# Optimization experiments

Measured on AMD Instinct MI355X. Metric: run time of the kernel, lower is better.

The kernel has to match this reference:

```python
import jax, jax.numpy as jnp
import numpy as np

U, V = 208, 176  # hard-coded DFT output shape from the original DFT2D
B, C, KH, KW = 32, 8, 3, 3


def dft2d(p):
    """Faithful vectorization of the original nested-loop DFT2D.
    dft[l, k] = (1/(M*N)) * sum_{m,n} p[m,n] * exp(-2j*pi*(k*m/V + l*n/U)),
    output shape (U, V) = (208, 176). Note the (intentionally) non-standard
    normalization axes, copied exactly from the source.
    """
    M, N = p.shape
    km = jnp.outer(jnp.arange(V), jnp.arange(M)).astype(jnp.float32)  # (V, M)
    ln = jnp.outer(jnp.arange(U), jnp.arange(N)).astype(jnp.float32)  # (U, N)
    E1 = jnp.exp(-2j * jnp.pi * km / V)  # (V, M) complex64
    E2 = jnp.exp(-2j * jnp.pi * ln / U)  # (U, N) complex64
    return jnp.einsum('km,mn,ln->lk', E1, p.astype(jnp.complex64), E2) / (M * N)


def setup_inputs() -> dict:
    key = jax.random.key(0)
    k1, k2 = jax.random.split(key)
    x = jax.random.normal(k1, (B, C, U, V), dtype=jnp.float32)
    kernel = jax.random.normal(k2, (KH, KW, 1, 1), dtype=jnp.float32)
    bias = jnp.zeros((1,), dtype=jnp.float32)
    return {"x": x, "kernel": kernel, "bias": bias}


def reference(x, kernel, bias):
    # Build the symmetric spatial kernel: [[k, flip_h(k)], [flip_w(k), flip_hw(k)]]
    k2 = kernel[::-1, :, :, :]
    k3 = kernel[:, ::-1, :, :]
    k4 = kernel[::-1, ::-1, :, :]
    sk = jnp.concatenate([jnp.concatenate([kernel, k2], axis=0),
                          jnp.concatenate([k3, k4], axis=0)], axis=1)  # (2KH, 2KW, 1, 1)
    sk2d = sk[:, :, 0, 0]  # tf.squeeze -> (2KH, 2KW)

    # k-space representation of the kernel and 50th-percentile binary mask
    fft_k = dft2d(sk2d)  # (208, 176) complex
    r = jnp.real(fft_k)
    thr = jnp.percentile(r, 50.0, method='nearest')  # tfp.stats.percentile default
    mask = (r > thr).astype(jnp.float32)  # (208, 176)

    # FFT of the image over its innermost two dims, mask in k-space, inverse FFT
    fft_x = jnp.fft.fft2(x)  # (B, C, 208, 176) complex64
    out = jnp.abs(jnp.fft.ifft2(fft_x * mask))  # bias unused on the test path
    return out
```

## Files before the change

kernel.cpp:

```cpp
#include <hip/hip_runtime.h>
#include <math.h>

#define UU 208
#define VV 176
#define NPIX (UU*VV)
#define ROWBLKS 1664

typedef __attribute__((ext_vector_type(2))) float v2f;
typedef __attribute__((ext_vector_type(4))) float v4f;

__device__ __forceinline__ v2f mk2(float x, float y){ v2f r; r.x = x; r.y = y; return r; }
__device__ __forceinline__ v2f sp(float s){ v2f r; r.x = s; r.y = s; return r; }

template<bool INV>
__device__ __forceinline__ v2f cmulc(v2f a, float wx, float wy_fwd){
  const float wy = INV ? -wy_fwd : wy_fwd;
  return sp(a.x) * mk2(wx, wy) + sp(a.y) * mk2(-wy, wx);
}
__device__ __forceinline__ v2f cmulw4(v2f a, v4f t){
  return sp(a.x) * mk2(t.x, t.y) + sp(a.y) * mk2(t.z, t.w);
}
__device__ __forceinline__ v2f cmulw4i(v2f a, v4f t){
  return sp(a.x) * mk2(t.x, t.z) + sp(a.y) * mk2(t.y, t.w);
}

template<bool INV>
__device__ __forceinline__ void dft4(v2f& x0, v2f& x1, v2f& x2, v2f& x3){
  v2f s0 = x0 + x2, d0 = x0 - x2;
  v2f s1 = x1 + x3, d1 = x1 - x3;
  v2f jd1;
  if (INV){ jd1.x = -d1.y; jd1.y =  d1.x; }
  else    { jd1.x =  d1.y; jd1.y = -d1.x; }
  x0 = s0 + s1; x2 = s0 - s1;
  x1 = d0 + jd1; x3 = d0 - jd1;
}

template<bool INV>
__device__ __forceinline__ void fft16(v2f v[16]){
  dft4<INV>(v[0], v[4], v[8],  v[12]);
  dft4<INV>(v[1], v[5], v[9],  v[13]);
  dft4<INV>(v[2], v[6], v[10], v[14]);
  dft4<INV>(v[3], v[7], v[11], v[15]);
  const float C1 = 0.92387953251128674f;
  const float S1 = 0.38268343236508978f;
  const float R2 = 0.70710678118654752f;
  v[5]  = cmulc<INV>(v[5],  C1, -S1);
  v[9]  = cmulc<INV>(v[9],  R2, -R2);
  v[13] = cmulc<INV>(v[13], S1, -C1);
  v[6]  = cmulc<INV>(v[6],  R2, -R2);
  v[10] = cmulc<INV>(v[10], 0.f, -1.f);
  v[14] = cmulc<INV>(v[14], -R2, -R2);
  v[7]  = cmulc<INV>(v[7],  S1, -C1);
  v[11] = cmulc<INV>(v[11], -R2, -R2);
  v[15] = cmulc<INV>(v[15], -C1,  S1);
  dft4<INV>(v[0],  v[1],  v[2],  v[3]);
  dft4<INV>(v[4],  v[5],  v[6],  v[7]);
  dft4<INV>(v[8],  v[9],  v[10], v[11]);
  dft4<INV>(v[12], v[13], v[14], v[15]);
}

template<int N, bool INV>
__device__ __forceinline__ void dftN(const v2f* __restrict__ t, v2f* __restrict__ F,
                                     const v2f* __restrict__ cs){
  v2f a = t[0];
  #pragma unroll
  for (int n = 1; n < N; n++) a += t[n];
  F[0] = a;
  #pragma unroll
  for (int k = 1; k <= N/2; k++){
    v2f C = t[0], S = sp(0.f);
    #pragma unroll
    for (int n = 1; n < N; n++){
      const int idx = (n * k) % N;
      C += t[n] * sp(cs[idx].x);
      S += t[n] * sp(cs[idx].y);
    }
    v2f ssw; ssw.x = S.y; ssw.y = -S.x;
    if (!INV){ F[k] = C + ssw; F[N-k] = C - ssw; }
    else     { F[k] = C - ssw; F[N-k] = C + ssw; }
  }
}

__device__ __forceinline__ unsigned sortable(float f){
  unsigned u = __float_as_uint(f);
  return (u & 0x80000000u) ? ~u : (u | 0x80000000u);
}

__device__ __forceinline__ unsigned find_bucket(const unsigned* __restrict__ bins_g,
                                                unsigned* sWS, unsigned* sB, unsigned* sK){
  const int t = threadIdx.x, lane = t & 63, wv = t >> 6;
  unsigned c = bins_g[t];
  unsigned v = c;
  #pragma unroll
  for (int d = 1; d < 64; d <<= 1){
    unsigned u = __shfl_up(v, d, 64);
    if (lane >= d) v += u;
  }
  if (lane == 63) sWS[wv] = v;
  __syncthreads();
  unsigned woff = 0;
  #pragma unroll
  for (int j = 0; j < 3; j++) woff += (j < wv) ? sWS[j] : 0u;
  unsigned incl = v + woff, excl = incl - c;
  unsigned k = *sK;
  __syncthreads();
  if (k >= excl && k < incl){ *sB = (unsigned)t; *sK = k - excl; }
  __syncthreads();
  return *sB;
}

__global__ __launch_bounds__(256) void rowfft_mask(const float* __restrict__ x, v2f* __restrict__ freq,
                                                   const float* __restrict__ kin, float* __restrict__ rbuf,
                                                   unsigned* __restrict__ bins24){
  const double PI2 = 6.283185307179586476925286766559;
  __shared__ v4f wf[VV];
  __shared__ v2f cs11[11];
  __shared__ v2f mid[16][177];
  if (blockIdx.x >= ROWBLKS){
    unsigned* h = (unsigned*)mid;
    h[threadIdx.x] = 0u;
    int i = (blockIdx.x - ROWBLKS) * 256 + threadIdx.x;
    int l = i / VV, k = i - l * VV;
    double c1, s1, c2, s2;
    { double a = PI2 * (double)k / (double)VV; c1 = cos(a); s1 = sin(a); }
    { double a = PI2 * (double)l / (double)UU; c2 = cos(a); s2 = sin(a); }
    double cA[6], sA[6], cB[6], sB[6];
    cA[0] = 1.0; sA[0] = 0.0; cA[1] = c1; sA[1] = s1;
    cB[0] = 1.0; sB[0] = 0.0; cB[1] = c2; sB[1] = s2;
    #pragma unroll
    for (int m = 2; m < 6; m++){
      cA[m] = 2.0*c1*cA[m-1] - cA[m-2];
      sA[m] = 2.0*c1*sA[m-1] - sA[m-2];
      cB[m] = 2.0*c2*cB[m-1] - cB[m-2];
      sB[m] = 2.0*c2*sB[m-1] - sB[m-2];
    }
    const int rm[6] = {0, 1, 2, 2, 1, 0};
    double P[3], Q[3];
    #pragma unroll
    for (int a = 0; a < 3; a++){
      P[a] = 0.0; Q[a] = 0.0;
      #pragma unroll
      for (int n = 0; n < 6; n++){
        double kv = (double)kin[a*3 + rm[n]];
        P[a] += kv * cB[n];
        Q[a] += kv * sB[n];
      }
    }
    double s = 0.0;
    #pragma unroll
    for (int m = 0; m < 6; m++)
      s += cA[m]*P[rm[m]] - sA[m]*Q[rm[m]];
    float val = (float)(s / 36.0);
    rbuf[i] = val;
    __syncthreads();
    atomicAdd(&h[sortable(val) >> 24], 1u);
    __syncthreads();
    if (h[threadIdx.x]) atomicAdd(&bins24[threadIdx.x], h[threadIdx.x]);
    return;
  }
  { int i = threadIdx.x;
    if (i < VV){
      double a = -PI2 * (double)i / (double)VV;
      float c = (float)cos(a), s = (float)sin(a);
      v4f f; f.x = c; f.y = s; f.z = -s; f.w = c; wf[i] = f;
    }
    if (i < 11){
      double a = PI2 * (double)i / 11.0;
      cs11[i] = mk2((float)cos(a), (float)sin(a));
    } }
  const int gr = threadIdx.x >> 4, ln = threadIdx.x & 15;
  const int row = blockIdx.x * 16 + gr;
  const int p = row / UU, rr = row - p * UU;
  const float* xr1 = x + ((size_t)(2*p) * UU + rr) * VV;
  const float* xr2 = xr1 + (size_t)NPIX;
  v2f* fr = freq + (size_t)row * VV;
  __syncthreads();
  if (ln < 11){
    v2f v[16];
    #pragma unroll
    for (int a = 0; a < 16; a++) v[a] = mk2(xr1[11*a + ln], xr2[11*a + ln]);
    fft16<false>(v);
    #pragma unroll
    for (int j = 0; j < 16; j++)
      mid[gr][j*11 + ln] = cmulw4(v[4*(j&3) + (j>>2)], wf[ln*j]);
  }
  v2f t[11], F[11];
  #pragma unroll
  for (int n2 = 0; n2 < 11; n2++) t[n2] = mid[gr][ln*11 + n2];
  dftN<11,false>(t, F, cs11);
  #pragma unroll
  for (int k2 = 0; k2 < 11; k2++) fr[ln + 16*k2] = F[k2];
}

template<int LEVEL>
__global__ __launch_bounds__(256) void hist_pass(const float* __restrict__ rbuf,
                                                 const unsigned* __restrict__ binsAll,
                                                 unsigned* __restrict__ binsOut){
  __shared__ unsigned h[256];
  __shared__ unsigned sWS[4];
  __shared__ unsigned sB, sK;
  if (threadIdx.x == 0) sK = 18304u;
  h[threadIdx.x] = 0u;
  __syncthreads();
  unsigned prefix = find_bucket(binsAll, sWS, &sB, &sK) << 24;
  if (LEVEL >= 2) prefix |= find_bucket(binsAll + 256, sWS, &sB, &sK) << 16;
  if (LEVEL >= 3) prefix |= find_bucket(binsAll + 512, sWS, &sB, &sK) << 8;
  const int SHIFT = 24 - 8*LEVEL;
  int i = blockIdx.x * 256 + threadIdx.x;
  unsigned u = sortable(rbuf[i]);
  if ((u >> (SHIFT + 8)) == (prefix >> (SHIFT + 8)))
    atomicAdd(&h[(u >> SHIFT) & 255u], 1u);
  __syncthreads();
  if (h[threadIdx.x]) atomicAdd(&binsOut[threadIdx.x], h[threadIdx.x]);
}

__global__ __launch_bounds__(256) void thr_final(const unsigned* __restrict__ binsAll,
                                                 float* __restrict__ thrOut){
  __shared__ unsigned sWS[4];
  __shared__ unsigned sB, sK;
  if (threadIdx.x == 0) sK = 18304u;
  __syncthreads();
  unsigned prefix = find_bucket(binsAll,       sWS, &sB, &sK) << 24;
  prefix |= find_bucket(binsAll + 256, sWS, &sB, &sK) << 16;
  prefix |= find_bucket(binsAll + 512, sWS, &sB, &sK) << 8;
  prefix |= find_bucket(binsAll + 768, sWS, &sB, &sK);
  if (threadIdx.x == 0){
    unsigned u = prefix;
    u = (u & 0x80000000u) ? (u ^ 0x80000000u) : ~u;
    thrOut[0] = __uint_as_float(u);
  }
}

__global__ __launch_bounds__(256) void colfft(v2f* __restrict__ freq,
                                              const float* __restrict__ rbuf, const float* __restrict__ thrp){
  __shared__ v4f wf[UU];
  __shared__ v2f cs13[13];
  __shared__ v2f buf[UU*17];
  { int i = threadIdx.x;
    const double PI2 = 6.283185307179586476925286766559;
    if (i < UU){
      double a = -PI2 * (double)i / (double)UU;
      float c = (float)cos(a), s = (float)sin(a);
      v4f f; f.x = c; f.y = s; f.z = -s; f.w = c; wf[i] = f;
    }
    if (i < 13){
      double a = PI2 * (double)i / 13.0;
      cs13[i] = mk2((float)cos(a), (float)sin(a));
    } }
  const int role = threadIdx.x >> 4, c = threadIdx.x & 15;
  const int img = blockIdx.x / 11;
  const int v0 = (blockIdx.x - img*11) << 4;
  v2f* base = freq + (size_t)img * NPIX + v0 + c;
  const float thr = thrp[0];
  __syncthreads();
  if (role < 13){
    v2f v[16];
    #pragma unroll
    for (int a = 0; a < 16; a++) v[a] = base[(13*a + role)*VV];
    fft16<false>(v);
    #pragma unroll
    for (int j = 0; j < 16; j++)
      buf[(j*13 + role)*17 + c] = cmulw4(v[4*(j&3) + (j>>2)], wf[role*j]);
  }
  __syncthreads();
  v2f F[13];
  {
    v2f t[13];
    #pragma unroll
    for (int n2 = 0; n2 < 13; n2++) t[n2] = buf[(role*13 + n2)*17 + c];
    dftN<13,false>(t, F, cs13);
    #pragma unroll
    for (int k2 = 0; k2 < 13; k2++){
      int u = role + 16*k2;
      float m = (rbuf[u*VV + v0 + c] > thr) ? 1.0f : 0.0f;
      F[k2] *= sp(m);
    }
  }
  __syncthreads();
  #pragma unroll
  for (int k2 = 0; k2 < 13; k2++) buf[(role + 16*k2)*17 + c] = F[k2];
  __syncthreads();
  if (role < 13){
    v2f v[16];
    #pragma unroll
    for (int a = 0; a < 16; a++) v[a] = buf[(13*a + role)*17 + c];
    fft16<true>(v);
    #pragma unroll
    for (int j = 0; j < 16; j++)
      buf[(j*13 + role)*17 + c] = cmulw4i(v[4*(j&3) + (j>>2)], wf[role*j]);
  }
  __syncthreads();
  {
    v2f t[13], G[13];
    #pragma unroll
    for (int n2 = 0; n2 < 13; n2++) t[n2] = buf[(role*13 + n2)*17 + c];
    dftN<13,true>(t, G, cs13);
    #pragma unroll
    for (int k2 = 0; k2 < 13; k2++)
      base[(role + 16*k2)*VV] = G[k2];
  }
}

__global__ __launch_bounds__(256) void rowifft_abs(const v2f* __restrict__ freq, float* __restrict__ out){
  __shared__ v4f wf[VV];
  __shared__ v2f cs11[11];
  __shared__ v2f mid[16][177];
  { int i = threadIdx.x;
    const double PI2 = 6.283185307179586476925286766559;
    if (i < VV){
      double a = -PI2 * (double)i / (double)VV;
      float c = (float)cos(a), s = (float)sin(a);
      v4f f; f.x = c; f.y = s; f.z = -s; f.w = c; wf[i] = f;
    }
    if (i < 11){
      double a = PI2 * (double)i / 11.0;
      cs11[i] = mk2((float)cos(a), (float)sin(a));
    } }
  const int gr = threadIdx.x >> 4, ln = threadIdx.x & 15;
  const int row = blockIdx.x * 16 + gr;
  const int p = row / UU, rr = row - p * UU;
  const v2f* fr = freq + (size_t)row * VV;
  float* orow1 = out + ((size_t)(2*p) * UU + rr) * VV;
  float* orow2 = orow1 + (size_t)NPIX;
  __syncthreads();
  if (ln < 11){
    v2f v[16];
    #pragma unroll
    for (int a = 0; a < 16; a++) v[a] = fr[11*a + ln];
    fft16<true>(v);
    #pragma unroll
    for (int j = 0; j < 16; j++)
      mid[gr][j*11 + ln] = cmulw4i(v[4*(j&3) + (j>>2)], wf[ln*j]);
  }
  v2f t[11], G[11];
  #pragma unroll
  for (int n2 = 0; n2 < 11; n2++) t[n2] = mid[gr][ln*11 + n2];
  dftN<11,true>(t, G, cs11);
  #pragma unroll
  for (int k2 = 0; k2 < 11; k2++){
    orow1[ln + 16*k2] = fabsf(G[k2].x) * (1.0f / 36608.0f);
    orow2[ln + 16*k2] = fabsf(G[k2].y) * (1.0f / 36608.0f);
  }
}

extern "C" void kernel_launch(void* const* d_in, const int* in_sizes, int n_in,
                              void* d_out, int out_size, void* d_ws, size_t ws_size,
                              hipStream_t stream){
  const float* x   = (const float*)d_in[0];
  const float* kin = (const float*)d_in[1];
  float* out = (float*)d_out;
  char* ws = (char*)d_ws;
  v2f*      freq = (v2f*)ws;
  float*    rbuf = (float*)(ws + 37486592);
  float*    thr  = (float*)(ws + 37633024);
  unsigned* bins = (unsigned*)(ws + 37633040);

  hipMemsetAsync(bins, 0, 4*256*4, stream);
  hipLaunchKernelGGL(rowfft_mask,  dim3(ROWBLKS + 143), dim3(256), 0, stream, x, freq, kin, rbuf, bins);
  hipLaunchKernelGGL(hist_pass<1>, dim3(143),           dim3(256), 0, stream, rbuf, bins, bins + 256);
  hipLaunchKernelGGL(hist_pass<2>, dim3(143),           dim3(256), 0, stream, rbuf, bins, bins + 512);
  hipLaunchKernelGGL(hist_pass<3>, dim3(143),           dim3(256), 0, stream, rbuf, bins, bins + 768);
  hipLaunchKernelGGL(thr_final,    dim3(1),             dim3(256), 0, stream, bins, thr);
  hipLaunchKernelGGL(colfft,       dim3(1408),          dim3(256), 0, stream, freq, rbuf, thr);
  hipLaunchKernelGGL(rowifft_abs,  dim3(1664),          dim3(256), 0, stream, freq, out);
}
```

Baseline: 72.62 us.

## Fuse percentile radix-select passes into row FFT kernel via grid barrier

Moves the mask-threshold computation into the first 143 blocks of the row-FFT kernel. Those blocks run a three-level 11/11/10-bit radix select, separated by spin-wait grid barriers on a global counter, instead of three histogram kernels plus a final kernel. This removes four kernel launches and their serialization gaps. The cost is spin-waiting blocks and larger shared histograms. It relies on all 143 mask blocks being co-resident, which holds when they are scheduled first.

```diff
diff --git a/kernel.cpp b/kernel.cpp
--- a/kernel.cpp
+++ b/kernel.cpp
@@ -4,6 +4,7 @@
 #define UU 208
 #define VV 176
 #define NPIX (UU*VV)
+#define MASKBLKS 143
 #define ROWBLKS 1664
 
 typedef __attribute__((ext_vector_type(2))) float v2f;
@@ -86,11 +87,28 @@
   return (u & 0x80000000u) ? ~u : (u | 0x80000000u);
 }
 
-__device__ __forceinline__ unsigned find_bucket(const unsigned* __restrict__ bins_g,
-                                                unsigned* sWS, unsigned* sB, unsigned* sK){
+__device__ __forceinline__ void mask_barrier(unsigned* counter, unsigned target){
+  __syncthreads();
+  if (threadIdx.x == 0){
+    __threadfence();
+    __hip_atomic_fetch_add(counter, 1u, __ATOMIC_ACQ_REL, __HIP_MEMORY_SCOPE_AGENT);
+    while (__hip_atomic_load(counter, __ATOMIC_ACQUIRE, __HIP_MEMORY_SCOPE_AGENT) < target)
+      __builtin_amdgcn_s_sleep(2);
+  }
+  __syncthreads();
+}
+
+template<int PER>
+__device__ __forceinline__ unsigned findNk(const unsigned* __restrict__ bins_g,
+                                           unsigned* sWS, unsigned* sRes, unsigned* kRef){
   const int t = threadIdx.x, lane = t & 63, wv = t >> 6;
-  unsigned c = bins_g[t];
-  unsigned v = c;
+  unsigned c[PER]; unsigned s = 0;
+  #pragma unroll
+  for (int j = 0; j < PER; j++){
+    c[j] = __hip_atomic_load(&bins_g[t*PER + j], __ATOMIC_RELAXED, __HIP_MEMORY_SCOPE_AGENT);
+    s += c[j];
+  }
+  unsigned v = s;
   #pragma unroll
   for (int d = 1; d < 64; d <<= 1){
     unsigned u = __shfl_up(v, d, 64);
@@ -101,25 +119,37 @@
   unsigned woff = 0;
   #pragma unroll
   for (int j = 0; j < 3; j++) woff += (j < wv) ? sWS[j] : 0u;
-  unsigned incl = v + woff, excl = incl - c;
-  unsigned k = *sK;
-  __syncthreads();
-  if (k >= excl && k < incl){ *sB = (unsigned)t; *sK = k - excl; }
-  __syncthreads();
-  return *sB;
+  unsigned incl = v + woff, excl = incl - s;
+  unsigned k = *kRef;
+  if (k >= excl && k < incl){
+    unsigned kk = k - excl; unsigned b = (unsigned)(t*PER);
+    #pragma unroll
+    for (int j = 0; j < PER; j++){
+      if (kk < c[j]){ b = (unsigned)(t*PER + j); break; }
+      kk -= c[j];
+    }
+    sRes[0] = b; sRes[1] = kk;
+  }
+  __syncthreads();
+  *kRef = sRes[1];
+  unsigned b = sRes[0];
+  __syncthreads();
+  return b;
 }
 
 __global__ __launch_bounds__(256) void rowfft_mask(const float* __restrict__ x, v2f* __restrict__ freq,
                                                    const float* __restrict__ kin, float* __restrict__ rbuf,
-                                                   unsigned* __restrict__ bins24){
+                                                   unsigned* __restrict__ bins0, unsigned* __restrict__ bins1,
+                                                   unsigned* __restrict__ bins2, unsigned* __restrict__ counter,
+                                                   float* __restrict__ thrOut){
   const double PI2 = 6.283185307179586476925286766559;
   __shared__ v4f wf[VV];
   __shared__ v2f cs11[11];
   __shared__ v2f mid[16][177];
-  if (blockIdx.x >= ROWBLKS){
-    unsigned* h = (unsigned*)mid;
-    h[threadIdx.x] = 0u;
-    int i = (blockIdx.x - ROWBLKS) * 256 + threadIdx.x;
+  __shared__ unsigned sWS[4], sRes[2];
+  if (blockIdx.x < MASKBLKS){
+    unsigned* h = (unsigned*)&mid[0][0];
+    int i = blockIdx.x * 256 + threadIdx.x;
     int l = i / VV, k = i - l * VV;
     double c1, s1, c2, s2;
     { double a = PI2 * (double)k / (double)VV; c1 = cos(a); s1 = sin(a); }
@@ -152,10 +182,49 @@
       s += cA[m]*P[rm[m]] - sA[m]*Q[rm[m]];
     float val = (float)(s / 36.0);
     rbuf[i] = val;
-    __syncthreads();
-    atomicAdd(&h[sortable(val) >> 24], 1u);
-    __syncthreads();
-    if (h[threadIdx.x]) atomicAdd(&bins24[threadIdx.x], h[threadIdx.x]);
+    const unsigned uval = sortable(val);
+    #pragma unroll
+    for (int j = 0; j < 8; j++) h[threadIdx.x*8 + j] = 0u;
+    __syncthreads();
+    atomicAdd(&h[uval >> 21], 1u);
+    __syncthreads();
+    #pragma unroll
+    for (int j = 0; j < 8; j++){
+      unsigned hv = h[threadIdx.x*8 + j];
+      if (hv) atomicAdd(&bins0[threadIdx.x*8 + j], hv);
+    }
+    mask_barrier(counter, MASKBLKS);
+    unsigned kk = 18304u;
+    unsigned b0 = findNk<8>(bins0, sWS, sRes, &kk);
+    #pragma unroll
+    for (int j = 0; j < 8; j++) h[threadIdx.x*8 + j] = 0u;
+    __syncthreads();
+    if ((uval >> 21) == b0) atomicAdd(&h[(uval >> 10) & 2047u], 1u);
+    __syncthreads();
+    #pragma unroll
+    for (int j = 0; j < 8; j++){
+      unsigned hv = h[threadIdx.x*8 + j];
+      if (hv) atomicAdd(&bins1[threadIdx.x*8 + j], hv);
+    }
+    mask_barrier(counter, 2u*MASKBLKS);
+    unsigned b1 = findNk<8>(bins1, sWS, sRes, &kk);
+    #pragma unroll
+    for (int j = 0; j < 4; j++) h[threadIdx.x*4 + j] = 0u;
+    __syncthreads();
+    if ((uval >> 10) == ((b0 << 11) | b1)) atomicAdd(&h[uval & 1023u], 1u);
+    __syncthreads();
+    #pragma unroll
+    for (int j = 0; j < 4; j++){
+      unsigned hv = h[threadIdx.x*4 + j];
+      if (hv) atomicAdd(&bins2[threadIdx.x*4 + j], hv);
+    }
+    mask_barrier(counter, 3u*MASKBLKS);
+    unsigned b2 = findNk<4>(bins2, sWS, sRes, &kk);
+    if (blockIdx.x == 0 && threadIdx.x == 0){
+      unsigned u = (b0 << 21) | (b1 << 10) | b2;
+      u = (u & 0x80000000u) ? (u ^ 0x80000000u) : ~u;
+      thrOut[0] = __uint_as_float(u);
+    }
     return;
   }
   { int i = threadIdx.x;
@@ -169,7 +238,7 @@
       cs11[i] = mk2((float)cos(a), (float)sin(a));
     } }
   const int gr = threadIdx.x >> 4, ln = threadIdx.x & 15;
-  const int row = blockIdx.x * 16 + gr;
+  const int row = (blockIdx.x - MASKBLKS) * 16 + gr;
   const int p = row / UU, rr = row - p * UU;
   const float* xr1 = x + ((size_t)(2*p) * UU + rr) * VV;
   const float* xr2 = xr1 + (size_t)NPIX;
@@ -190,45 +259,6 @@
   dftN<11,false>(t, F, cs11);
   #pragma unroll
   for (int k2 = 0; k2 < 11; k2++) fr[ln + 16*k2] = F[k2];
-}
-
-template<int LEVEL>
-__global__ __launch_bounds__(256) void hist_pass(const float* __restrict__ rbuf,
-                                                 const unsigned* __restrict__ binsAll,
-                                                 unsigned* __restrict__ binsOut){
-  __shared__ unsigned h[256];
-  __shared__ unsigned sWS[4];
-  __shared__ unsigned sB, sK;
-  if (threadIdx.x == 0) sK = 18304u;
-  h[threadIdx.x] = 0u;
-  __syncthreads();
-  unsigned prefix = find_bucket(binsAll, sWS, &sB, &sK) << 24;
-  if (LEVEL >= 2) prefix |= find_bucket(binsAll + 256, sWS, &sB, &sK) << 16;
-  if (LEVEL >= 3) prefix |= find_bucket(binsAll + 512, sWS, &sB, &sK) << 8;
-  const int SHIFT = 24 - 8*LEVEL;
-  int i = blockIdx.x * 256 + threadIdx.x;
-  unsigned u = sortable(rbuf[i]);
-  if ((u >> (SHIFT + 8)) == (prefix >> (SHIFT + 8)))
-    atomicAdd(&h[(u >> SHIFT) & 255u], 1u);
-  __syncthreads();
-  if (h[threadIdx.x]) atomicAdd(&binsOut[threadIdx.x], h[threadIdx.x]);
-}
-
-__global__ __launch_bounds__(256) void thr_final(const unsigned* __restrict__ binsAll,
-                                                 float* __restrict__ thrOut){
-  __shared__ unsigned sWS[4];
-  __shared__ unsigned sB, sK;
-  if (threadIdx.x == 0) sK = 18304u;
-  __syncthreads();
-  unsigned prefix = find_bucket(binsAll,       sWS, &sB, &sK) << 24;
-  prefix |= find_bucket(binsAll + 256, sWS, &sB, &sK) << 16;
-  prefix |= find_bucket(binsAll + 512, sWS, &sB, &sK) << 8;
-  prefix |= find_bucket(binsAll + 768, sWS, &sB, &sK);
-  if (threadIdx.x == 0){
-    unsigned u = prefix;
-    u = (u & 0x80000000u) ? (u ^ 0x80000000u) : ~u;
-    thrOut[0] = __uint_as_float(u);
-  }
 }
 
 __global__ __launch_bounds__(256) void colfft(v2f* __restrict__ freq,
@@ -350,17 +380,17 @@
   const float* kin = (const float*)d_in[1];
   float* out = (float*)d_out;
   char* ws = (char*)d_ws;
-  v2f*      freq = (v2f*)ws;
-  float*    rbuf = (float*)(ws + 37486592);
-  float*    thr  = (float*)(ws + 37633024);
-  unsigned* bins = (unsigned*)(ws + 37633040);
-
-  hipMemsetAsync(bins, 0, 4*256*4, stream);
-  hipLaunchKernelGGL(rowfft_mask,  dim3(ROWBLKS + 143), dim3(256), 0, stream, x, freq, kin, rbuf, bins);
-  hipLaunchKernelGGL(hist_pass<1>, dim3(143),           dim3(256), 0, stream, rbuf, bins, bins + 256);
-  hipLaunchKernelGGL(hist_pass<2>, dim3(143),           dim3(256), 0, stream, rbuf, bins, bins + 512);
-  hipLaunchKernelGGL(hist_pass<3>, dim3(143),           dim3(256), 0, stream, rbuf, bins, bins + 768);
-  hipLaunchKernelGGL(thr_final,    dim3(1),             dim3(256), 0, stream, bins, thr);
-  hipLaunchKernelGGL(colfft,       dim3(1408),          dim3(256), 0, stream, freq, rbuf, thr);
-  hipLaunchKernelGGL(rowifft_abs,  dim3(1664),          dim3(256), 0, stream, freq, out);
-}
+  v2f*      freq  = (v2f*)ws;
+  float*    rbuf  = (float*)(ws + 37486592);
+  float*    thr   = (float*)(ws + 37633024);
+  unsigned* bins0 = (unsigned*)(ws + 37633040);
+  unsigned* bins1 = bins0 + 2048;
+  unsigned* bins2 = bins1 + 2048;
+  unsigned* counter = bins2 + 1024;
+
+  hipMemsetAsync(bins0, 0, (2048 + 2048 + 1024 + 4) * 4, stream);
+  hipLaunchKernelGGL(rowfft_mask, dim3(MASKBLKS + ROWBLKS), dim3(256), 0, stream,
+                     x, freq, kin, rbuf, bins0, bins1, bins2, counter, thr);
+  hipLaunchKernelGGL(colfft,      dim3(1408), dim3(256), 0, stream, freq, rbuf, thr);
+  hipLaunchKernelGGL(rowifft_abs, dim3(1664), dim3(256), 0, stream, freq, out);
+}
```

New measurement: 111.9 us. +54.1%, slower.
